# Kernel optimization log

Hardware: AMD Instinct MI355X
Metric: run time of the kernel (lower is better)

The kernel has to match this reference:

```python
import jax, jax.numpy as jnp
import numpy as np

B, L, D2, C = 64, 512, 512, 50  # D2 = hidden_size*2

def setup_inputs() -> dict:
    key = jax.random.key(0)
    ks = jax.random.split(key, 8)
    text_vec = jax.random.normal(ks[0], (B, L, D2), dtype=jnp.float32)
    text_mask = jnp.ones((B, L), dtype=bool)
    sbj_bound = jnp.sort(jax.random.randint(ks[1], (B, 2), 0, L), axis=-1)
    obj_start = jax.random.randint(ks[2], (B, L), 0, C)
    obj_end = jax.random.randint(ks[3], (B, L), 0, C)
    W_start = jax.random.normal(ks[4], (2 * D2, C), dtype=jnp.float32) * 0.02
    b_start = jnp.zeros((C,), dtype=jnp.float32)
    W_end = jax.random.normal(ks[5], (2 * D2, C), dtype=jnp.float32) * 0.02
    b_end = jnp.zeros((C,), dtype=jnp.float32)
    return {"text_vec": text_vec, "text_mask": text_mask, "sbj_bound": sbj_bound,
            "obj_start": obj_start, "obj_end": obj_end,
            "W_start": W_start, "b_start": b_start, "W_end": W_end, "b_end": b_end}

def _masked_ce(logits, labels, maskf, value_num):
    # logits [B,L,C], labels [B,L]
    logp = jax.nn.log_softmax(logits, axis=-1)
    nll = -jnp.take_along_axis(logp, labels[..., None], axis=-1)[..., 0]
    return (nll * maskf).sum() / value_num

def reference(text_vec, text_mask, sbj_bound, obj_start, obj_end,
              W_start, b_start, W_end, b_end):
    pos = jnp.arange(L)  # [L]
    start, end = sbj_bound[:, 0], sbj_bound[:, 1]
    # inclusive span mask, vectorized replacement for the per-example loop
    span = ((pos[None, :] >= start[:, None]) & (pos[None, :] <= end[:, None])).astype(text_vec.dtype)  # [B,L]
    count = span.sum(axis=1, keepdims=True)  # [B,1], >=1 since start<=end
    sbj_vec = jnp.einsum('bl,bld->bd', span, text_vec) / count  # segment mean [B,D2]
    # cat([text_vec, sbj_vec]) @ W  ==  text_vec @ W[:D2] + sbj_vec @ W[D2:]
    def head(W, b):
        return (jnp.einsum('bld,dc->blc', text_vec, W[:D2])
                + (sbj_vec @ W[D2:])[:, None, :] + b)
    o1 = head(W_start, b_start)
    o2 = head(W_end, b_end)
    maskf = text_mask.astype(jnp.float32)
    value_num = maskf.sum()
    loss_obj_s = _masked_ce(o1, obj_start, maskf, value_num)
    loss_obj_e = _masked_ce(o2, obj_end, maskf, value_num)
    return loss_obj_s + loss_obj_e
```

## Files before the change

### kernel.cpp

```cpp
#include <hip/hip_runtime.h>
#include <math.h>

#define BB 64
#define LL 512
#define DD 512
#define CC 50
#define NC 100
#define NCP 112

#define WSB_LOSS  0
#define WSB_CNT   4
#define WSB_DONE  8
#define WSB_SCOMB 64
#define WSB_PART  28736
#define WSB_WBOT  553024
#define WSB_BPACK 667712

typedef __attribute__((ext_vector_type(8))) short bf16x8;
typedef __attribute__((ext_vector_type(4))) float f32x4;

static __device__ __forceinline__ unsigned short f2bf(float x) {
    unsigned int u = __float_as_uint(x);
    u += 0x7FFFu + ((u >> 16) & 1u);
    return (unsigned short)(u >> 16);
}
static __device__ __forceinline__ float bf2f(unsigned short h) {
    return __uint_as_float(((unsigned int)h) << 16);
}
static __device__ __forceinline__ unsigned int pk2bf(float a, float b) {
    return __builtin_amdgcn_perm(__float_as_uint(b), __float_as_uint(a), 0x07060302u);
}
static __device__ __forceinline__ void gl2lds16(const void* g, void* l) {
    __builtin_amdgcn_global_load_lds(
        (const __attribute__((address_space(1))) unsigned int*)g,
        (__attribute__((address_space(3))) unsigned int*)l, 16, 0, 0);
}

__global__ __launch_bounds__(256) void k_prep(
    const float* __restrict__ tv, const int* __restrict__ sbj_bound,
    const float* __restrict__ Wst, const float* __restrict__ Wen,
    char* __restrict__ wsb)
{
    __shared__ float sh[128 * 53];
    const int t = threadIdx.x;
    const int blk = blockIdx.x;

    if (blk < 512) {
        const int b = blk >> 3, seg = blk & 7;
        const int start = sbj_bound[2 * b], end = sbj_bound[2 * b + 1];
        int r0 = seg * 64;      if (r0 < start) r0 = start;
        int r1 = seg * 64 + 63; if (r1 > end)   r1 = end;
        const int c4 = t & 127, par = t >> 7;
        const float* bp = tv + (size_t)b * LL * DD + c4 * 4;
        float4 a0 = {0, 0, 0, 0}, a1 = {0, 0, 0, 0};
        int r = r0 + par;
        for (; r + 2 <= r1; r += 4) {
            float4 v0 = *(const float4*)(bp + (size_t)r * DD);
            float4 v1 = *(const float4*)(bp + (size_t)(r + 2) * DD);
            a0.x += v0.x; a0.y += v0.y; a0.z += v0.z; a0.w += v0.w;
            a1.x += v1.x; a1.y += v1.y; a1.z += v1.z; a1.w += v1.w;
        }
        for (; r <= r1; r += 2) {
            float4 v0 = *(const float4*)(bp + (size_t)r * DD);
            a0.x += v0.x; a0.y += v0.y; a0.z += v0.z; a0.w += v0.w;
        }
        float4* buf = (float4*)sh;
        float4 acc = {a0.x + a1.x, a0.y + a1.y, a0.z + a1.z, a0.w + a1.w};
        buf[t] = acc;
        __syncthreads();
        if (t < 128) {
            float4 x = buf[t], y = buf[t + 128];
            unsigned short* part = (unsigned short*)(wsb + WSB_PART);
            ushort4 o;
            o.x = f2bf(x.x + y.x); o.y = f2bf(x.y + y.y);
            o.z = f2bf(x.z + y.z); o.w = f2bf(x.w + y.w);
            *(ushort4*)(part + ((size_t)(seg * BB + b)) * DD + t * 4) = o;
        }
    } else if (blk < 520) {
        const int bi = blk - 512;
        const int mat = bi >> 2;
        const int cj = bi & 3;
        const float* W = mat ? Wen : Wst;
        const int kbase = 512 + cj * 128;
        const float* src = W + (size_t)kbase * CC;
#pragma unroll
        for (int i = 0; i < 25; i++) {
            int idx = t + i * 256;
            sh[idx] = src[idx];
        }
        __syncthreads();
        unsigned short* outp = (unsigned short*)(wsb + WSB_WBOT);
        const int kout = cj * 128;
#pragma unroll
        for (int i = 0; i < 25; i++) {
            int idx = t + i * 256;
            int n = idx >> 7, kl = idx & 127;
            outp[((size_t)(mat * CC + n)) * DD + kout + kl] = f2bf(sh[kl * 50 + n]);
        }
        if (bi == 0 && t == 0) {
            *(float*)(wsb + WSB_LOSS) = 0.0f;
            *(float*)(wsb + WSB_CNT)  = 0.0f;
            *(int*)(wsb + WSB_DONE)   = 0;
        }
    } else {
        const int bi = blk - 520;
        const int ln = t & 63, jj = t >> 6;
        const int tc = ln & 15, quad = ln >> 4;
        const int j0 = jj * 2;
        unsigned int* bp = (unsigned int*)(wsb + WSB_BPACK);
#pragma unroll
        for (int q = 0; q < 7; q++) {
            const int fid = bi * 7 + q;
            const int u = fid % 7, s = fid / 7;
            const int cc = u * 16 + tc;
            const int k0 = s * 32 + quad * 8 + j0;
            float a = 0.f, bb = 0.f;
            if (cc < CC) {
                a  = Wst[(size_t)k0 * CC + cc];
                bb = Wst[(size_t)(k0 + 1) * CC + cc];
            } else if (cc < NC) {
                a  = Wen[(size_t)k0 * CC + cc - CC];
                bb = Wen[(size_t)(k0 + 1) * CC + cc - CC];
            }
            bp[fid * 256 + ln * 4 + jj] =
                (unsigned int)f2bf(a) | ((unsigned int)f2bf(bb) << 16);
        }
    }
}

#define SST 520
__global__ __launch_bounds__(256) void k_scomb(
    const int* __restrict__ sbj_bound,
    const float* __restrict__ bst, const float* __restrict__ ben,
    char* __restrict__ wsb)
{
    __shared__ __align__(16) unsigned short sbjb[16 * SST];
    const int t = threadIdx.x;
    const int g = blockIdx.x;
    const unsigned short* part = (const unsigned short*)(wsb + WSB_PART);

#pragma unroll
    for (int i = 0; i < 8; i++) {
        int idx = t + i * 256;
        int bo = idx >> 7, d4 = idx & 127;
        int b = g * 16 + bo;
        float inv = 1.0f / (float)(sbj_bound[2 * b + 1] - sbj_bound[2 * b] + 1);
        float sx = 0.f, sy = 0.f, sz = 0.f, sw = 0.f;
#pragma unroll
        for (int seg = 0; seg < 8; seg++) {
            ushort4 v = *(const ushort4*)(part + ((size_t)(seg * BB + b)) * DD + d4 * 4);
            sx += bf2f(v.x); sy += bf2f(v.y); sz += bf2f(v.z); sw += bf2f(v.w);
        }
        ushort4 o;
        o.x = f2bf(sx * inv); o.y = f2bf(sy * inv);
        o.z = f2bf(sz * inv); o.w = f2bf(sw * inv);
        *(ushort4*)(sbjb + bo * SST + d4 * 4) = o;
    }
    __syncthreads();

    const int wv = t >> 6, ln = t & 63, tc = ln & 15, quad = ln >> 4;
    const unsigned short* wbot = (const unsigned short*)(wsb + WSB_WBOT);
    float* scomb = (float*)(wsb + WSB_SCOMB);
    const unsigned short* Af = sbjb + tc * SST + quad * 8;
    const int nu = (wv < 3) ? 2 : 1;
    for (int j = 0; j < nu; j++) {
        const int u = wv * 2 + j;
        f32x4 acc = (f32x4)(0.0f);
        const unsigned short* Bf = wbot + (size_t)(u * 16 + tc) * DD + quad * 8;
#pragma unroll
        for (int kk = 0; kk < DD; kk += 32) {
            bf16x8 af = *(const bf16x8*)(Af + kk);
            bf16x8 bf = *(const bf16x8*)(Bf + kk);
            acc = __builtin_amdgcn_mfma_f32_16x16x32_bf16(af, bf, acc, 0, 0, 0);
        }
        const int cc = u * 16 + tc;
        const float bias = (cc < CC) ? bst[cc] : ((cc < NC) ? ben[cc - CC] : 0.0f);
#pragma unroll
        for (int i = 0; i < 4; i++) {
            int b = g * 16 + quad * 4 + i;
            scomb[b * NCP + cc] = acc[i] + bias;
        }
    }
}

__global__ __launch_bounds__(256, 1) void k_main(
    const float* __restrict__ tv,
    const int* __restrict__ mask,
    const int* __restrict__ obj_s, const int* __restrict__ obj_e,
    char* __restrict__ wsb, float* __restrict__ out)
{
    __shared__ __align__(16) unsigned short Bl[112 * 512];
    __shared__ float red[8];
    const int t = threadIdx.x, wv = t >> 6, ln = t & 63;
    const int tc = ln & 15, quad = ln >> 4;
    const int m0 = blockIdx.x * 64;
    const int b = blockIdx.x >> 3;

    const float* Ap = tv + (size_t)(m0 + wv * 16 + tc) * DD + quad * 8;

    float4 ra0[8], ra1[8];
#pragma unroll
    for (int ks = 0; ks < 4; ks++) {
        ra0[2 * ks]     = *(const float4*)(Ap + ks * 32);
        ra0[2 * ks + 1] = *(const float4*)(Ap + ks * 32 + 4);
    }
#pragma unroll
    for (int ks = 0; ks < 4; ks++) {
        ra1[2 * ks]     = *(const float4*)(Ap + (4 + ks) * 32);
        ra1[2 * ks + 1] = *(const float4*)(Ap + (4 + ks) * 32 + 4);
    }
    {
        const char* gB = wsb + WSB_BPACK;
#pragma unroll
        for (int i = 0; i < 28; i++) {
            const int gidx = t + i * 256;
            gl2lds16(gB + (size_t)gidx * 16,
                     (char*)Bl + (i * 256 + wv * 64) * 16);
        }
    }
    __syncthreads();

    f32x4 acc[7];
#pragma unroll
    for (int u = 0; u < 7; u++) acc[u] = (f32x4)(0.0f);
    const unsigned short* Bf0 = Bl + ln * 8;

#pragma unroll
    for (int bt = 0; bt < 4; bt++) {
        float4* cur = (bt & 1) ? ra1 : ra0;
#pragma unroll
        for (int ks = 0; ks < 4; ks++) {
            const int s = bt * 4 + ks;
            float4 v0 = cur[2 * ks], v1 = cur[2 * ks + 1];
            union { unsigned int u32[4]; bf16x8 v; } af;
            af.u32[0] = pk2bf(v0.x, v0.y);
            af.u32[1] = pk2bf(v0.z, v0.w);
            af.u32[2] = pk2bf(v1.x, v1.y);
            af.u32[3] = pk2bf(v1.z, v1.w);
#pragma unroll
            for (int u = 0; u < 7; u++) {
                bf16x8 bf = *(const bf16x8*)(Bf0 + (s * 7 + u) * 512);
                acc[u] = __builtin_amdgcn_mfma_f32_16x16x32_bf16(af.v, bf, acc[u], 0, 0, 0);
            }
        }
        if (bt < 2) {
#pragma unroll
            for (int ks = 0; ks < 4; ks++) {
                cur[2 * ks]     = *(const float4*)(Ap + (4 * (bt + 2) + ks) * 32);
                cur[2 * ks + 1] = *(const float4*)(Ap + (4 * (bt + 2) + ks) * 32 + 4);
            }
        }
    }

    const float* scomb = (const float*)(wsb + WSB_SCOMB);
    float sc[7];
#pragma unroll
    for (int u = 0; u < 7; u++) sc[u] = scomb[b * NCP + u * 16 + tc];

    float loss_local = 0.0f, cnt_local = 0.0f;
#pragma unroll
    for (int i = 0; i < 4; i++) {
        const int l = (m0 + wv * 16 + quad * 4 + i) & (LL - 1);
        const int lab1 = obj_s[b * LL + l];
        const int lab2 = obj_e[b * LL + l] + CC;
        const int mk   = mask[b * LL + l];
        float lg[7];
#pragma unroll
        for (int u = 0; u < 7; u++) lg[u] = acc[u][i] + sc[u];
        float m1 = fmaxf(fmaxf(lg[0], lg[1]), lg[2]);
        if (tc < 2) m1 = fmaxf(m1, lg[3]);
        float m2 = fmaxf(lg[4], lg[5]);
        if (tc >= 2) m2 = fmaxf(m2, lg[3]);
        if (tc < 4)  m2 = fmaxf(m2, lg[6]);
#pragma unroll
        for (int off = 1; off < 16; off <<= 1) {
            m1 = fmaxf(m1, __shfl_xor(m1, off, 16));
            m2 = fmaxf(m2, __shfl_xor(m2, off, 16));
        }
        float e1 = expf(lg[0] - m1) + expf(lg[1] - m1) + expf(lg[2] - m1)
                 + ((tc < 2) ? expf(lg[3] - m1) : 0.0f);
        float e2 = expf(lg[4] - m2) + expf(lg[5] - m2)
                 + ((tc >= 2) ? expf(lg[3] - m2) : 0.0f)
                 + ((tc < 4)  ? expf(lg[6] - m2) : 0.0f);
        float t1 = 0.0f, t2 = 0.0f;
#pragma unroll
        for (int u = 0; u < 7; u++) {
            const int cc = u * 16 + tc;
            if (cc == lab1) t1 = lg[u];
            if (cc == lab2) t2 = lg[u];
        }
#pragma unroll
        for (int off = 1; off < 16; off <<= 1) {
            e1 += __shfl_xor(e1, off, 16);
            e2 += __shfl_xor(e2, off, 16);
            t1 += __shfl_xor(t1, off, 16);
            t2 += __shfl_xor(t2, off, 16);
        }
        if (tc == 0) {
            const float nll = (m1 + logf(e1) - t1) + (m2 + logf(e2) - t2);
            loss_local += mk ? nll : 0.0f;
            cnt_local  += mk ? 1.0f : 0.0f;
        }
    }
#pragma unroll
    for (int off = 1; off < 64; off <<= 1) {
        loss_local += __shfl_xor(loss_local, off);
        cnt_local  += __shfl_xor(cnt_local, off);
    }
    if (ln == 0) { red[wv * 2] = loss_local; red[wv * 2 + 1] = cnt_local; }
    __syncthreads();
    if (t == 0) {
        float Ls = red[0] + red[2] + red[4] + red[6];
        float Cs = red[1] + red[3] + red[5] + red[7];
        float* wsf = (float*)wsb;
        atomicAdd(&wsf[0], Ls);
        atomicAdd(&wsf[1], Cs);
        __threadfence();
        int old = atomicAdd((int*)(wsb + WSB_DONE), 1);
        if (old == (int)gridDim.x - 1) {
            float L = atomicAdd(&wsf[0], 0.0f);
            float C = atomicAdd(&wsf[1], 0.0f);
            out[0] = L / C;
        }
    }
}

extern "C" void kernel_launch(void* const* d_in, const int* in_sizes, int n_in,
                              void* d_out, int out_size, void* d_ws, size_t ws_size,
                              hipStream_t stream) {
    const float* tv   = (const float*)d_in[0];
    const int*   mask = (const int*)d_in[1];
    const int*   sbj  = (const int*)d_in[2];
    const int*   objs = (const int*)d_in[3];
    const int*   obje = (const int*)d_in[4];
    const float* Wst  = (const float*)d_in[5];
    const float* bst  = (const float*)d_in[6];
    const float* Wen  = (const float*)d_in[7];
    const float* ben  = (const float*)d_in[8];
    float* out = (float*)d_out;
    char*  wsb = (char*)d_ws;

    k_prep<<<536, 256, 0, stream>>>(tv, sbj, Wst, Wen, wsb);
    k_scomb<<<4, 256, 0, stream>>>(sbj, bst, ben, wsb);
    k_main<<<512, 256, 0, stream>>>(tv, mask, objs, obje, wsb, out);
}
```

Measured before the change: 154.0 us.

## Double row tile per block and stream A through swizzled LDS double buffer

Each block of k_main now handles 128 rows instead of 64, with each wave computing two 16-row MFMA tiles that share every B fragment read from LDS. The grid drops from 512 to 256 blocks, so the packed weight matrix is copied into LDS half as many times. Activation rows are no longer loaded into registers; they are streamed through a per-wave, XOR-swizzled LDS ping-pong buffer with async global-to-LDS copies issued two K-steps ahead. In exchange, fewer blocks than CUs (256 blocks) may leave parts of the GPU idle, and the extra accumulators plus about 32KB more LDS raise register and LDS pressure.

After: 145.2 us. -5.7%, faster.

```diff
diff --git a/kernel.cpp b/kernel.cpp
--- a/kernel.cpp
+++ b/kernel.cpp
@@ -190,65 +190,66 @@
     char* __restrict__ wsb, float* __restrict__ out)
 {
     __shared__ __align__(16) unsigned short Bl[112 * 512];
+    __shared__ __align__(16) float Aw[4 * 2 * 1024];
     __shared__ float red[8];
     const int t = threadIdx.x, wv = t >> 6, ln = t & 63;
     const int tc = ln & 15, quad = ln >> 4;
-    const int m0 = blockIdx.x * 64;
-    const int b = blockIdx.x >> 3;
-
-    const float* Ap = tv + (size_t)(m0 + wv * 16 + tc) * DD + quad * 8;
-
-    float4 ra0[8], ra1[8];
-#pragma unroll
-    for (int ks = 0; ks < 4; ks++) {
-        ra0[2 * ks]     = *(const float4*)(Ap + ks * 32);
-        ra0[2 * ks + 1] = *(const float4*)(Ap + ks * 32 + 4);
-    }
-#pragma unroll
-    for (int ks = 0; ks < 4; ks++) {
-        ra1[2 * ks]     = *(const float4*)(Ap + (4 + ks) * 32);
-        ra1[2 * ks + 1] = *(const float4*)(Ap + (4 + ks) * 32 + 4);
-    }
+    const int m0 = blockIdx.x * 128;
+    const int wr0 = m0 + wv * 32;
+    const int b = blockIdx.x >> 2;
+
+    const int rl = ln >> 3;
+    const int gsw = (ln & 7) ^ rl;
+    const float* asrc = tv + (size_t)(wr0 + rl) * DD + gsw * 4;
+    float* Asl0 = Aw + wv * 2048;
+    float* Asl1 = Aw + wv * 2048 + 1024;
+
     {
         const char* gB = wsb + WSB_BPACK;
 #pragma unroll
         for (int i = 0; i < 28; i++) {
             const int gidx = t + i * 256;
-            gl2lds16(gB + (size_t)gidx * 16,
-                     (char*)Bl + (i * 256 + wv * 64) * 16);
-        }
-    }
+            gl2lds16(gB + (size_t)gidx * 16, (char*)Bl + (i * 256 + wv * 64) * 16);
+        }
+    }
+#pragma unroll
+    for (int j = 0; j < 4; j++)
+        gl2lds16(asrc + (size_t)j * 8 * DD, (char*)(Asl0 + j * 256));
+#pragma unroll
+    for (int j = 0; j < 4; j++)
+        gl2lds16(asrc + (size_t)j * 8 * DD + 32, (char*)(Asl1 + j * 256));
     __syncthreads();
 
-    f32x4 acc[7];
-#pragma unroll
-    for (int u = 0; u < 7; u++) acc[u] = (f32x4)(0.0f);
+    f32x4 acc0[7], acc1[7];
+#pragma unroll
+    for (int u = 0; u < 7; u++) { acc0[u] = (f32x4)(0.0f); acc1[u] = (f32x4)(0.0f); }
     const unsigned short* Bf0 = Bl + ln * 8;
-
-#pragma unroll
-    for (int bt = 0; bt < 4; bt++) {
-        float4* cur = (bt & 1) ? ra1 : ra0;
-#pragma unroll
-        for (int ks = 0; ks < 4; ks++) {
-            const int s = bt * 4 + ks;
-            float4 v0 = cur[2 * ks], v1 = cur[2 * ks + 1];
-            union { unsigned int u32[4]; bf16x8 v; } af;
-            af.u32[0] = pk2bf(v0.x, v0.y);
-            af.u32[1] = pk2bf(v0.z, v0.w);
-            af.u32[2] = pk2bf(v1.x, v1.y);
-            af.u32[3] = pk2bf(v1.z, v1.w);
-#pragma unroll
-            for (int u = 0; u < 7; u++) {
-                bf16x8 bf = *(const bf16x8*)(Bf0 + (s * 7 + u) * 512);
-                acc[u] = __builtin_amdgcn_mfma_f32_16x16x32_bf16(af.v, bf, acc[u], 0, 0, 0);
-            }
-        }
-        if (bt < 2) {
-#pragma unroll
-            for (int ks = 0; ks < 4; ks++) {
-                cur[2 * ks]     = *(const float4*)(Ap + (4 * (bt + 2) + ks) * 32);
-                cur[2 * ks + 1] = *(const float4*)(Ap + (4 * (bt + 2) + ks) * 32 + 4);
-            }
+    const int R0 = tc, R1 = 16 + tc;
+    const int x0 = (quad * 2) ^ (tc & 7), x1 = (quad * 2 + 1) ^ (tc & 7);
+
+#pragma unroll
+    for (int s = 0; s < 16; s++) {
+        float* Asl = (s & 1) ? Asl1 : Asl0;
+        float4 v00 = *(const float4*)(Asl + R0 * 32 + x0 * 4);
+        float4 v01 = *(const float4*)(Asl + R0 * 32 + x1 * 4);
+        float4 v10 = *(const float4*)(Asl + R1 * 32 + x0 * 4);
+        float4 v11 = *(const float4*)(Asl + R1 * 32 + x1 * 4);
+        if (s < 14) {
+#pragma unroll
+            for (int j = 0; j < 4; j++)
+                gl2lds16(asrc + (size_t)j * 8 * DD + (s + 2) * 32,
+                         (char*)(Asl + j * 256));
+        }
+        union { unsigned int u32[4]; bf16x8 v; } af0, af1;
+        af0.u32[0] = pk2bf(v00.x, v00.y); af0.u32[1] = pk2bf(v00.z, v00.w);
+        af0.u32[2] = pk2bf(v01.x, v01.y); af0.u32[3] = pk2bf(v01.z, v01.w);
+        af1.u32[0] = pk2bf(v10.x, v10.y); af1.u32[1] = pk2bf(v10.z, v10.w);
+        af1.u32[2] = pk2bf(v11.x, v11.y); af1.u32[3] = pk2bf(v11.z, v11.w);
+#pragma unroll
+        for (int u = 0; u < 7; u++) {
+            bf16x8 bf = *(const bf16x8*)(Bf0 + (s * 7 + u) * 512);
+            acc0[u] = __builtin_amdgcn_mfma_f32_16x16x32_bf16(af0.v, bf, acc0[u], 0, 0, 0);
+            acc1[u] = __builtin_amdgcn_mfma_f32_16x16x32_bf16(af1.v, bf, acc1[u], 0, 0, 0);
         }
     }
 
@@ -259,47 +260,51 @@
 
     float loss_local = 0.0f, cnt_local = 0.0f;
 #pragma unroll
-    for (int i = 0; i < 4; i++) {
-        const int l = (m0 + wv * 16 + quad * 4 + i) & (LL - 1);
-        const int lab1 = obj_s[b * LL + l];
-        const int lab2 = obj_e[b * LL + l] + CC;
-        const int mk   = mask[b * LL + l];
-        float lg[7];
-#pragma unroll
-        for (int u = 0; u < 7; u++) lg[u] = acc[u][i] + sc[u];
-        float m1 = fmaxf(fmaxf(lg[0], lg[1]), lg[2]);
-        if (tc < 2) m1 = fmaxf(m1, lg[3]);
-        float m2 = fmaxf(lg[4], lg[5]);
-        if (tc >= 2) m2 = fmaxf(m2, lg[3]);
-        if (tc < 4)  m2 = fmaxf(m2, lg[6]);
-#pragma unroll
-        for (int off = 1; off < 16; off <<= 1) {
-            m1 = fmaxf(m1, __shfl_xor(m1, off, 16));
-            m2 = fmaxf(m2, __shfl_xor(m2, off, 16));
-        }
-        float e1 = expf(lg[0] - m1) + expf(lg[1] - m1) + expf(lg[2] - m1)
-                 + ((tc < 2) ? expf(lg[3] - m1) : 0.0f);
-        float e2 = expf(lg[4] - m2) + expf(lg[5] - m2)
-                 + ((tc >= 2) ? expf(lg[3] - m2) : 0.0f)
-                 + ((tc < 4)  ? expf(lg[6] - m2) : 0.0f);
-        float t1 = 0.0f, t2 = 0.0f;
-#pragma unroll
-        for (int u = 0; u < 7; u++) {
-            const int cc = u * 16 + tc;
-            if (cc == lab1) t1 = lg[u];
-            if (cc == lab2) t2 = lg[u];
-        }
-#pragma unroll
-        for (int off = 1; off < 16; off <<= 1) {
-            e1 += __shfl_xor(e1, off, 16);
-            e2 += __shfl_xor(e2, off, 16);
-            t1 += __shfl_xor(t1, off, 16);
-            t2 += __shfl_xor(t2, off, 16);
-        }
-        if (tc == 0) {
-            const float nll = (m1 + logf(e1) - t1) + (m2 + logf(e2) - t2);
-            loss_local += mk ? nll : 0.0f;
-            cnt_local  += mk ? 1.0f : 0.0f;
+    for (int mt = 0; mt < 2; mt++) {
+        f32x4* acc = mt ? acc1 : acc0;
+#pragma unroll
+        for (int i = 0; i < 4; i++) {
+            const int l = (wr0 + mt * 16 + quad * 4 + i) & (LL - 1);
+            const int lab1 = obj_s[b * LL + l];
+            const int lab2 = obj_e[b * LL + l] + CC;
+            const int mk   = mask[b * LL + l];
+            float lg[7];
+#pragma unroll
+            for (int u = 0; u < 7; u++) lg[u] = acc[u][i] + sc[u];
+            float m1 = fmaxf(fmaxf(lg[0], lg[1]), lg[2]);
+            if (tc < 2) m1 = fmaxf(m1, lg[3]);
+            float m2 = fmaxf(lg[4], lg[5]);
+            if (tc >= 2) m2 = fmaxf(m2, lg[3]);
+            if (tc < 4)  m2 = fmaxf(m2, lg[6]);
+#pragma unroll
+            for (int off = 1; off < 16; off <<= 1) {
+                m1 = fmaxf(m1, __shfl_xor(m1, off, 16));
+                m2 = fmaxf(m2, __shfl_xor(m2, off, 16));
+            }
+            float e1 = expf(lg[0] - m1) + expf(lg[1] - m1) + expf(lg[2] - m1)
+                     + ((tc < 2) ? expf(lg[3] - m1) : 0.0f);
+            float e2 = expf(lg[4] - m2) + expf(lg[5] - m2)
+                     + ((tc >= 2) ? expf(lg[3] - m2) : 0.0f)
+                     + ((tc < 4)  ? expf(lg[6] - m2) : 0.0f);
+            float t1 = 0.0f, t2 = 0.0f;
+#pragma unroll
+            for (int u = 0; u < 7; u++) {
+                const int cc = u * 16 + tc;
+                if (cc == lab1) t1 = lg[u];
+                if (cc == lab2) t2 = lg[u];
+            }
+#pragma unroll
+            for (int off = 1; off < 16; off <<= 1) {
+                e1 += __shfl_xor(e1, off, 16);
+                e2 += __shfl_xor(e2, off, 16);
+                t1 += __shfl_xor(t1, off, 16);
+                t2 += __shfl_xor(t2, off, 16);
+            }
+            if (tc == 0) {
+                const float nll = (m1 + logf(e1) - t1) + (m2 + logf(e2) - t2);
+                loss_local += mk ? nll : 0.0f;
+                cnt_local  += mk ? 1.0f : 0.0f;
+            }
         }
     }
 #pragma unroll
@@ -342,5 +347,5 @@
 
     k_prep<<<536, 256, 0, stream>>>(tv, sbj, Wst, Wen, wsb);
     k_scomb<<<4, 256, 0, stream>>>(sbj, bst, ben, wsb);
-    k_main<<<512, 256, 0, stream>>>(tv, mask, objs, obje, wsb, out);
-}
+    k_main<<<256, 256, 0, stream>>>(tv, mask, objs, obje, wsb, out);
+}
```

## Restructure main GEMM: waves split by N, B in registers, A staged via LDS

Applied to the files above, without the earlier changes.

Each block now runs 7 waves, one per 16-column slice of the 112 output classes. Each wave holds its B fragments in registers, while the 64x512 activation tile is streamed through a double-buffered, XOR-swizzled LDS buffer instead of per-wave register prefetch. Logits are written to shared memory and a row-per-thread softmax/CE computes the loss, replacing the shuffle-heavy per-fragment reduction. This cuts the 112 KB LDS footprint so several blocks can share a CU. The cost is 16 block barriers per tile and a serial 50-class loop handled by only 128 threads.

After: 155.3 us. No clear change (+0.9%).

```diff
diff --git a/kernel.cpp b/kernel.cpp
--- a/kernel.cpp
+++ b/kernel.cpp
@@ -183,124 +183,100 @@
     }
 }
 
-__global__ __launch_bounds__(256, 1) void k_main(
+__global__ __launch_bounds__(448, 4) void k_main(
     const float* __restrict__ tv,
     const int* __restrict__ mask,
     const int* __restrict__ obj_s, const int* __restrict__ obj_e,
     char* __restrict__ wsb, float* __restrict__ out)
 {
-    __shared__ __align__(16) unsigned short Bl[112 * 512];
-    __shared__ float red[8];
+    __shared__ __align__(16) float smem[64 * 113];
+    __shared__ float red[16];
     const int t = threadIdx.x, wv = t >> 6, ln = t & 63;
     const int tc = ln & 15, quad = ln >> 4;
+    const int u = wv;
     const int m0 = blockIdx.x * 64;
     const int b = blockIdx.x >> 3;
 
-    const float* Ap = tv + (size_t)(m0 + wv * 16 + tc) * DD + quad * 8;
-
-    float4 ra0[8], ra1[8];
-#pragma unroll
-    for (int ks = 0; ks < 4; ks++) {
-        ra0[2 * ks]     = *(const float4*)(Ap + ks * 32);
-        ra0[2 * ks + 1] = *(const float4*)(Ap + ks * 32 + 4);
-    }
-#pragma unroll
-    for (int ks = 0; ks < 4; ks++) {
-        ra1[2 * ks]     = *(const float4*)(Ap + (4 + ks) * 32);
-        ra1[2 * ks + 1] = *(const float4*)(Ap + (4 + ks) * 32 + 4);
-    }
+    bf16x8 breg[16];
     {
         const char* gB = wsb + WSB_BPACK;
 #pragma unroll
-        for (int i = 0; i < 28; i++) {
-            const int gidx = t + i * 256;
-            gl2lds16(gB + (size_t)gidx * 16,
-                     (char*)Bl + (i * 256 + wv * 64) * 16);
+        for (int s = 0; s < 16; s++)
+            breg[s] = *(const bf16x8*)(gB + ((size_t)((s * 7 + u) * 64 + ln)) * 16);
+    }
+
+    const int arow = ln >> 3;
+    const int agr  = (ln & 7) ^ (arow & 7);
+
+    {
+        const float* gbase = tv + (size_t)m0 * DD;
+#pragma unroll
+        for (int j = wv; j < 8; j += 7) {
+            const float* g = gbase + (size_t)(j * 8 + arow) * DD + agr * 4;
+            gl2lds16(g, (char*)smem + (size_t)j * 1024);
+        }
+    }
+
+    f32x4 acc[4];
+#pragma unroll
+    for (int mf = 0; mf < 4; mf++) acc[mf] = (f32x4)(0.0f);
+    const int g0 = (quad * 2) ^ (tc & 7);
+    const int g1 = (quad * 2 + 1) ^ (tc & 7);
+
+    for (int s = 0; s < 16; s++) {
+        __syncthreads();
+        if (s < 15) {
+            const float* gbase = tv + (size_t)m0 * DD + (s + 1) * 32;
+            char* dst = (char*)smem + ((s + 1) & 1) * 8192;
+#pragma unroll
+            for (int j = wv; j < 8; j += 7) {
+                const float* g = gbase + (size_t)(j * 8 + arow) * DD + agr * 4;
+                gl2lds16(g, dst + (size_t)j * 1024);
+            }
+        }
+        const float* Ab = smem + (s & 1) * 2048;
+#pragma unroll
+        for (int mf = 0; mf < 4; mf++) {
+            const int r = mf * 16 + tc;
+            float4 v0 = *(const float4*)(Ab + r * 32 + g0 * 4);
+            float4 v1 = *(const float4*)(Ab + r * 32 + g1 * 4);
+            union { unsigned int u32[4]; bf16x8 v; } af;
+            af.u32[0] = pk2bf(v0.x, v0.y); af.u32[1] = pk2bf(v0.z, v0.w);
+            af.u32[2] = pk2bf(v1.x, v1.y); af.u32[3] = pk2bf(v1.z, v1.w);
+            acc[mf] = __builtin_amdgcn_mfma_f32_16x16x32_bf16(af.v, breg[s], acc[mf], 0, 0, 0);
         }
     }
     __syncthreads();
 
-    f32x4 acc[7];
-#pragma unroll
-    for (int u = 0; u < 7; u++) acc[u] = (f32x4)(0.0f);
-    const unsigned short* Bf0 = Bl + ln * 8;
-
-#pragma unroll
-    for (int bt = 0; bt < 4; bt++) {
-        float4* cur = (bt & 1) ? ra1 : ra0;
-#pragma unroll
-        for (int ks = 0; ks < 4; ks++) {
-            const int s = bt * 4 + ks;
-            float4 v0 = cur[2 * ks], v1 = cur[2 * ks + 1];
-            union { unsigned int u32[4]; bf16x8 v; } af;
-            af.u32[0] = pk2bf(v0.x, v0.y);
-            af.u32[1] = pk2bf(v0.z, v0.w);
-            af.u32[2] = pk2bf(v1.x, v1.y);
-            af.u32[3] = pk2bf(v1.z, v1.w);
-#pragma unroll
-            for (int u = 0; u < 7; u++) {
-                bf16x8 bf = *(const bf16x8*)(Bf0 + (s * 7 + u) * 512);
-                acc[u] = __builtin_amdgcn_mfma_f32_16x16x32_bf16(af.v, bf, acc[u], 0, 0, 0);
+    {
+        const float* scomb = (const float*)(wsb + WSB_SCOMB);
+        const float scv = scomb[b * NCP + u * 16 + tc];
+#pragma unroll
+        for (int mf = 0; mf < 4; mf++) {
+#pragma unroll
+            for (int i = 0; i < 4; i++) {
+                const int row = mf * 16 + quad * 4 + i;
+                smem[row * 113 + u * 16 + tc] = acc[mf][i] + scv;
             }
         }
-        if (bt < 2) {
-#pragma unroll
-            for (int ks = 0; ks < 4; ks++) {
-                cur[2 * ks]     = *(const float4*)(Ap + (4 * (bt + 2) + ks) * 32);
-                cur[2 * ks + 1] = *(const float4*)(Ap + (4 * (bt + 2) + ks) * 32 + 4);
-            }
-        }
-    }
-
-    const float* scomb = (const float*)(wsb + WSB_SCOMB);
-    float sc[7];
-#pragma unroll
-    for (int u = 0; u < 7; u++) sc[u] = scomb[b * NCP + u * 16 + tc];
+    }
+    __syncthreads();
 
     float loss_local = 0.0f, cnt_local = 0.0f;
-#pragma unroll
-    for (int i = 0; i < 4; i++) {
-        const int l = (m0 + wv * 16 + quad * 4 + i) & (LL - 1);
-        const int lab1 = obj_s[b * LL + l];
-        const int lab2 = obj_e[b * LL + l] + CC;
-        const int mk   = mask[b * LL + l];
-        float lg[7];
-#pragma unroll
-        for (int u = 0; u < 7; u++) lg[u] = acc[u][i] + sc[u];
-        float m1 = fmaxf(fmaxf(lg[0], lg[1]), lg[2]);
-        if (tc < 2) m1 = fmaxf(m1, lg[3]);
-        float m2 = fmaxf(lg[4], lg[5]);
-        if (tc >= 2) m2 = fmaxf(m2, lg[3]);
-        if (tc < 4)  m2 = fmaxf(m2, lg[6]);
-#pragma unroll
-        for (int off = 1; off < 16; off <<= 1) {
-            m1 = fmaxf(m1, __shfl_xor(m1, off, 16));
-            m2 = fmaxf(m2, __shfl_xor(m2, off, 16));
-        }
-        float e1 = expf(lg[0] - m1) + expf(lg[1] - m1) + expf(lg[2] - m1)
-                 + ((tc < 2) ? expf(lg[3] - m1) : 0.0f);
-        float e2 = expf(lg[4] - m2) + expf(lg[5] - m2)
-                 + ((tc >= 2) ? expf(lg[3] - m2) : 0.0f)
-                 + ((tc < 4)  ? expf(lg[6] - m2) : 0.0f);
-        float t1 = 0.0f, t2 = 0.0f;
-#pragma unroll
-        for (int u = 0; u < 7; u++) {
-            const int cc = u * 16 + tc;
-            if (cc == lab1) t1 = lg[u];
-            if (cc == lab2) t2 = lg[u];
-        }
-#pragma unroll
-        for (int off = 1; off < 16; off <<= 1) {
-            e1 += __shfl_xor(e1, off, 16);
-            e2 += __shfl_xor(e2, off, 16);
-            t1 += __shfl_xor(t1, off, 16);
-            t2 += __shfl_xor(t2, off, 16);
-        }
-        if (tc == 0) {
-            const float nll = (m1 + logf(e1) - t1) + (m2 + logf(e2) - t2);
-            loss_local += mk ? nll : 0.0f;
-            cnt_local  += mk ? 1.0f : 0.0f;
-        }
+    if (t < 128) {
+        const int row = t >> 1, head = t & 1;
+        const int l = (m0 + row) & (LL - 1);
+        const int lab = head ? obj_e[b * LL + l] : obj_s[b * LL + l];
+        const int mk  = mask[b * LL + l];
+        const float* Lr = smem + row * 113 + head * CC;
+        float mx = Lr[0];
+#pragma unroll 5
+        for (int c = 1; c < CC; c++) mx = fmaxf(mx, Lr[c]);
+        float es = 0.0f;
+#pragma unroll 5
+        for (int c = 0; c < CC; c++) es = __builtin_fmaf(expf(Lr[c] - mx), 1.0f, es);
+        const float nll = mx + logf(es) - Lr[lab];
+        if (mk) { loss_local = nll; cnt_local = head ? 0.0f : 1.0f; }
     }
 #pragma unroll
     for (int off = 1; off < 64; off <<= 1) {
@@ -310,8 +286,9 @@
     if (ln == 0) { red[wv * 2] = loss_local; red[wv * 2 + 1] = cnt_local; }
     __syncthreads();
     if (t == 0) {
-        float Ls = red[0] + red[2] + red[4] + red[6];
-        float Cs = red[1] + red[3] + red[5] + red[7];
+        float Ls = 0.f, Cs = 0.f;
+#pragma unroll
+        for (int w = 0; w < 7; w++) { Ls += red[w * 2]; Cs += red[w * 2 + 1]; }
         float* wsf = (float*)wsb;
         atomicAdd(&wsf[0], Ls);
         atomicAdd(&wsf[1], Cs);
@@ -342,5 +319,5 @@
 
     k_prep<<<536, 256, 0, stream>>>(tv, sbj, Wst, Wen, wsb);
     k_scomb<<<4, 256, 0, stream>>>(sbj, bst, ben, wsb);
-    k_main<<<512, 256, 0, stream>>>(tv, mask, objs, obje, wsb, out);
-}
+    k_main<<<512, 448, 0, stream>>>(tv, mask, objs, obje, wsb, out);
+}
```
